# Kernel optimization log

Hardware: AMD Instinct MI355X
Metric: run time of the kernel (lower is better)

The kernel has to match this reference:

```python
import jax, jax.numpy as jnp
import numpy as np


def _extract_patches(x, k):
    # tf.image.extract_patches(sizes=[1,k,k,1], strides=1, rates=1, padding='SAME')
    # reshaped to [B,H,W,k*k,C]; window ordered row-major (di, dj), zero padded.
    B, H, W, C = x.shape
    p = k // 2
    xp = jnp.pad(x, ((0, 0), (p, p), (p, p), (0, 0)))
    # fixed k*k=25 shifted views; stacking along new patch axis
    views = [xp[:, i:i + H, j:j + W, :] for i in range(k) for j in range(k)]
    return jnp.stack(views, axis=3)  # [B,H,W,k*k,C]


def reference(main, main_value, ref, ref_value, k_size=5):
    # main/ref: [B,H,W,C]; main_value/ref_value: [B,H,W,V]
    ref_p = _extract_patches(ref, k_size)            # [B,H,W,K,C], K=k*k
    refv_p = _extract_patches(ref_value, k_size)     # [B,H,W,K,V]

    # scores for the K neighbor slots plus one self slot (main concat at end)
    scores_nbr = jnp.einsum('bhwkc,bhwc->bhwk', ref_p, main)   # [B,H,W,K]
    score_self = jnp.einsum('bhwc,bhwc->bhw', main, main)      # [B,H,W]
    scores = jnp.concatenate([scores_nbr, score_self[..., None]], axis=-1)  # [B,H,W,K+1]

    attn = jax.nn.softmax(scores, axis=-1)                     # [B,H,W,K+1]

    values = jnp.concatenate([refv_p, main_value[:, :, :, None, :]], axis=3)  # [B,H,W,K+1,V]
    out = jnp.einsum('bhwk,bhwkv->bhwv', attn, values)         # [B,H,W,V]
    return out


def setup_inputs() -> dict:
    key = jax.random.key(0)
    k1, k2, k3, k4 = jax.random.split(key, 4)
    B, H, W, C, V = 2, 128, 128, 256, 64
    return {
        'main': jax.random.normal(k1, (B, H, W, C), dtype=jnp.float32),
        'main_value': jax.random.normal(k2, (B, H, W, V), dtype=jnp.float32),
        'ref': jax.random.normal(k3, (B, H, W, C), dtype=jnp.float32),
        'ref_value': jax.random.normal(k4, (B, H, W, V), dtype=jnp.float32),
    }
```

## Files before the change

### kernel.cpp

```cpp
#include <hip/hip_runtime.h>
#include <math.h>

namespace {

constexpr int Bn = 2, Hn = 128, Wn = 128, Cn = 256, Vn = 64;

__device__ __forceinline__ void load8(float* r, const float* p) {
    float4 a = *(const float4*)(p);
    float4 b = *(const float4*)(p + 4);
    r[0]=a.x; r[1]=a.y; r[2]=a.z; r[3]=a.w;
    r[4]=b.x; r[5]=b.y; r[6]=b.z; r[7]=b.w;
}

__global__ __launch_bounds__(256)
void local_attn_kernel(const float* __restrict__ mainp,
                       const float* __restrict__ mainv,
                       const float* __restrict__ refp,
                       const float* __restrict__ refv,
                       float* __restrict__ outp)
{
    const int t = threadIdx.x;
    const int s = t & 15;
    const int p = t >> 4;
    const int blk = blockIdx.x;
    const int seg = blk & 7;
    const int h   = (blk >> 3) & (Hn - 1);
    const int b   = blk >> 10;
    const int w   = seg * 16 + p;
    const int rowbase = b * Hn + h;

    float m[16];
    const float* mp = mainp + ((size_t)rowbase * Wn + w) * Cn + s * 8;
    load8(m,     mp);
    load8(m + 8, mp + 128);

    float self = 0.f;
    #pragma unroll
    for (int c = 0; c < 16; ++c) self = fmaf(m[c], m[c], self);
    self += __shfl_xor(self, 1);
    self += __shfl_xor(self, 2);
    self += __shfl_xor(self, 4);
    self += __shfl_xor(self, 8);

    float mx = self, den = 1.f;
    float acc[4];
    {
        const float* mvp = mainv + ((size_t)rowbase * Wn + w) * Vn + s * 4;
        float4 a = *(const float4*)(mvp);
        acc[0]=a.x; acc[1]=a.y; acc[2]=a.z; acc[3]=a.w;
    }

    #pragma unroll 1
    for (int di = 0; di < 5; ++di) {
        const int hh = h + di - 2;
        const bool rowok = (unsigned)hh < (unsigned)Hn;
        const size_t rbase = (size_t)(b * Hn + (rowok ? hh : 0)) * Wn;
        const float* rp = refp + rbase * Cn + s * 8;

        float sc[5] = {0.f, 0.f, 0.f, 0.f, 0.f};
        #pragma unroll
        for (int dj = 0; dj < 5; ++dj) {
            const int col = w - 2 + dj;
            const bool ok = rowok && (unsigned)col < (unsigned)Wn;
            float r[8];
            #pragma unroll
            for (int c = 0; c < 8; ++c) r[c] = 0.f;
            if (ok) load8(r, rp + (size_t)col * Cn);
            float a = 0.f;
            #pragma unroll
            for (int c = 0; c < 8; ++c) a = fmaf(m[c], r[c], a);
            sc[dj] = a;
        }
        #pragma unroll
        for (int dj = 0; dj < 5; ++dj) {
            const int col = w - 2 + dj;
            const bool ok = rowok && (unsigned)col < (unsigned)Wn;
            float r[8];
            #pragma unroll
            for (int c = 0; c < 8; ++c) r[c] = 0.f;
            if (ok) load8(r, rp + (size_t)col * Cn + 128);
            float a = sc[dj];
            #pragma unroll
            for (int c = 0; c < 8; ++c) a = fmaf(m[8 + c], r[c], a);
            sc[dj] = a;
        }

        #pragma unroll
        for (int k = 0; k < 5; ++k) {
            float v = sc[k];
            v += __shfl_xor(v, 1);
            v += __shfl_xor(v, 2);
            v += __shfl_xor(v, 4);
            v += __shfl_xor(v, 8);
            sc[k] = v;
        }

        const float rm = fmaxf(fmaxf(fmaxf(sc[0], sc[1]), fmaxf(sc[2], sc[3])), sc[4]);
        const float nm = fmaxf(mx, rm);
        const float e  = __expf(mx - nm);
        float wk[5];
        float sum = 0.f;
        #pragma unroll
        for (int k = 0; k < 5; ++k) { wk[k] = __expf(sc[k] - nm); sum += wk[k]; }
        den = den * e + sum;
        #pragma unroll
        for (int c = 0; c < 4; ++c) acc[c] *= e;
        mx = nm;

        const float* rvp = refv + rbase * Vn + s * 4;
        #pragma unroll
        for (int dj = 0; dj < 5; ++dj) {
            const int col = w - 2 + dj;
            float4 rv = make_float4(0.f, 0.f, 0.f, 0.f);
            if (rowok && (unsigned)col < (unsigned)Wn)
                rv = *(const float4*)(rvp + (size_t)col * Vn);
            const float wkj = wk[dj];
            acc[0] = fmaf(wkj, rv.x, acc[0]);
            acc[1] = fmaf(wkj, rv.y, acc[1]);
            acc[2] = fmaf(wkj, rv.z, acc[2]);
            acc[3] = fmaf(wkj, rv.w, acc[3]);
        }
    }

    const float inv = 1.f / den;
    float* op = outp + ((size_t)rowbase * Wn + w) * Vn + s * 4;
    float4 o;
    o.x = acc[0]*inv; o.y = acc[1]*inv; o.z = acc[2]*inv; o.w = acc[3]*inv;
    *(float4*)op = o;
}

}

extern "C" void kernel_launch(void* const* d_in, const int* in_sizes, int n_in,
                              void* d_out, int out_size, void* d_ws, size_t ws_size,
                              hipStream_t stream)
{
    const float* mainp = (const float*)d_in[0];
    const float* mainv = (const float*)d_in[1];
    const float* refp  = (const float*)d_in[2];
    const float* refv  = (const float*)d_in[3];
    float* outp = (float*)d_out;

    dim3 grid(Bn * Hn * 8);
    dim3 block(256);
    hipLaunchKernelGGL(local_attn_kernel, grid, block, 0, stream,
                       mainp, mainv, refp, refv, outp);
}
```

Before: 41.69 us.

## Fully unroll window rows and replace online softmax with two-pass softmax

Replaces the per-row online softmax loop (unroll 1) with a fully unrolled computation of all 25 scores first, followed by a single max/exp/sum pass and then the value accumulation. All reference loads for the whole 5x5 window can now be issued back to back, which gives more memory-level parallelism and removes the rescaling of the accumulator after each row. The cost is higher register pressure (25 scores plus many in-flight loads), which could lower occupancy under the 256-thread launch bound.

```diff
diff --git a/kernel.cpp b/kernel.cpp
--- a/kernel.cpp
+++ b/kernel.cpp
@@ -42,22 +42,12 @@
     self += __shfl_xor(self, 4);
     self += __shfl_xor(self, 8);
 
-    float mx = self, den = 1.f;
-    float acc[4];
-    {
-        const float* mvp = mainv + ((size_t)rowbase * Wn + w) * Vn + s * 4;
-        float4 a = *(const float4*)(mvp);
-        acc[0]=a.x; acc[1]=a.y; acc[2]=a.z; acc[3]=a.w;
-    }
-
-    #pragma unroll 1
+    float sc[25];
+    #pragma unroll
     for (int di = 0; di < 5; ++di) {
         const int hh = h + di - 2;
         const bool rowok = (unsigned)hh < (unsigned)Hn;
-        const size_t rbase = (size_t)(b * Hn + (rowok ? hh : 0)) * Wn;
-        const float* rp = refp + rbase * Cn + s * 8;
-
-        float sc[5] = {0.f, 0.f, 0.f, 0.f, 0.f};
+        const float* rp = refp + (size_t)(b * Hn + (rowok ? hh : 0)) * Wn * Cn + s * 8;
         #pragma unroll
         for (int dj = 0; dj < 5; ++dj) {
             const int col = w - 2 + dj;
@@ -69,8 +59,14 @@
             float a = 0.f;
             #pragma unroll
             for (int c = 0; c < 8; ++c) a = fmaf(m[c], r[c], a);
-            sc[dj] = a;
+            sc[di * 5 + dj] = a;
         }
+    }
+    #pragma unroll
+    for (int di = 0; di < 5; ++di) {
+        const int hh = h + di - 2;
+        const bool rowok = (unsigned)hh < (unsigned)Hn;
+        const float* rp = refp + (size_t)(b * Hn + (rowok ? hh : 0)) * Wn * Cn + s * 8;
         #pragma unroll
         for (int dj = 0; dj < 5; ++dj) {
             const int col = w - 2 + dj;
@@ -79,42 +75,51 @@
             #pragma unroll
             for (int c = 0; c < 8; ++c) r[c] = 0.f;
             if (ok) load8(r, rp + (size_t)col * Cn + 128);
-            float a = sc[dj];
+            float a = sc[di * 5 + dj];
             #pragma unroll
             for (int c = 0; c < 8; ++c) a = fmaf(m[8 + c], r[c], a);
-            sc[dj] = a;
+            sc[di * 5 + dj] = a;
         }
+    }
 
-        #pragma unroll
-        for (int k = 0; k < 5; ++k) {
-            float v = sc[k];
-            v += __shfl_xor(v, 1);
-            v += __shfl_xor(v, 2);
-            v += __shfl_xor(v, 4);
-            v += __shfl_xor(v, 8);
-            sc[k] = v;
-        }
+    #pragma unroll
+    for (int k = 0; k < 25; ++k) {
+        float v = sc[k];
+        v += __shfl_xor(v, 1);
+        v += __shfl_xor(v, 2);
+        v += __shfl_xor(v, 4);
+        v += __shfl_xor(v, 8);
+        sc[k] = v;
+    }
 
-        const float rm = fmaxf(fmaxf(fmaxf(sc[0], sc[1]), fmaxf(sc[2], sc[3])), sc[4]);
-        const float nm = fmaxf(mx, rm);
-        const float e  = __expf(mx - nm);
-        float wk[5];
-        float sum = 0.f;
-        #pragma unroll
-        for (int k = 0; k < 5; ++k) { wk[k] = __expf(sc[k] - nm); sum += wk[k]; }
-        den = den * e + sum;
-        #pragma unroll
-        for (int c = 0; c < 4; ++c) acc[c] *= e;
-        mx = nm;
+    float mx = self;
+    #pragma unroll
+    for (int k = 0; k < 25; ++k) mx = fmaxf(mx, sc[k]);
+    float den = __expf(self - mx);
+    const float wself = den;
+    #pragma unroll
+    for (int k = 0; k < 25; ++k) { sc[k] = __expf(sc[k] - mx); den += sc[k]; }
+    const float inv = 1.f / den;
 
-        const float* rvp = refv + rbase * Vn + s * 4;
+    float acc[4];
+    {
+        const float* mvp = mainv + ((size_t)rowbase * Wn + w) * Vn + s * 4;
+        float4 a = *(const float4*)(mvp);
+        acc[0] = wself * a.x; acc[1] = wself * a.y;
+        acc[2] = wself * a.z; acc[3] = wself * a.w;
+    }
+    #pragma unroll
+    for (int di = 0; di < 5; ++di) {
+        const int hh = h + di - 2;
+        const bool rowok = (unsigned)hh < (unsigned)Hn;
+        const float* rvp = refv + (size_t)(b * Hn + (rowok ? hh : 0)) * Wn * Vn + s * 4;
         #pragma unroll
         for (int dj = 0; dj < 5; ++dj) {
             const int col = w - 2 + dj;
             float4 rv = make_float4(0.f, 0.f, 0.f, 0.f);
             if (rowok && (unsigned)col < (unsigned)Wn)
                 rv = *(const float4*)(rvp + (size_t)col * Vn);
-            const float wkj = wk[dj];
+            const float wkj = sc[di * 5 + dj];
             acc[0] = fmaf(wkj, rv.x, acc[0]);
             acc[1] = fmaf(wkj, rv.y, acc[1]);
             acc[2] = fmaf(wkj, rv.z, acc[2]);
@@ -122,7 +127,6 @@
         }
     }
 
-    const float inv = 1.f / den;
     float* op = outp + ((size_t)rowbase * Wn + w) * Vn + s * 4;
     float4 o;
     o.x = acc[0]*inv; o.y = acc[1]*inv; o.z = acc[2]*inv; o.w = acc[3]*inv;
```

Result: slower. 65.88 us (+58.0%).
